# Optimization experiments

Measured on AMD Instinct MI355X. Metric: run time of the kernel, lower is better.

The kernel has to match this reference:

```python
import jax, jax.numpy as jnp
import numpy as np

B, N, D = 1, 768, 256
H = 4
HD = D // H
K = 16
EDGE_DIM = 4
LN_EPS = 1e-5


def setup_inputs() -> dict:
    key = jax.random.key(0)
    ks = jax.random.split(key, 16)
    g = lambda k, shape, fan: jax.random.normal(k, shape, jnp.float32) / np.sqrt(fan)
    return {
        'x': jax.random.normal(ks[0], (B, N, D), jnp.float32),
        'Wqkv_w': g(ks[1], (D, 3 * D), D), 'Wqkv_b': jnp.zeros((3 * D,), jnp.float32),
        'out_w': g(ks[2], (D, D), D), 'out_b': jnp.zeros((D,), jnp.float32),
        'ffn1_w': g(ks[3], (2 * D, 2 * D), 2 * D), 'ffn1_b': jnp.zeros((2 * D,), jnp.float32),
        'ln_g': jnp.ones((2 * D,), jnp.float32), 'ln_b': jnp.zeros((2 * D,), jnp.float32),
        'ffn2_w': g(ks[4], (2 * D, D), 2 * D), 'ffn2_b': jnp.zeros((D,), jnp.float32),
        'e1_w': g(ks[5], (EDGE_DIM, 2 * H), EDGE_DIM), 'e1_b': jnp.zeros((2 * H,), jnp.float32),
        'e2_w': g(ks[6], (2 * H, H), 2 * H), 'e2_b': jnp.zeros((H,), jnp.float32),
        'graph_gate': jnp.float32(0.5),
    }


def _normalize(v):
    return v / jnp.clip(jnp.linalg.norm(v, axis=-1, keepdims=True), 1e-12)


def reference(x, Wqkv_w, Wqkv_b, out_w, out_b, ffn1_w, ffn1_b, ln_g, ln_b,
              ffn2_w, ffn2_b, e1_w, e1_b, e2_w, e2_b, graph_gate):
    b, n, d = x.shape
    # ---- graph topology (no grad, discrete top-k) ----
    xs = jax.lax.stop_gradient(x)
    dn_s = _normalize(xs)
    sim_d = jnp.einsum('bnd,bmd->bnm', dn_s, dn_s)
    eye = jnp.eye(n, dtype=bool)
    sim_d = jnp.where(eye, -jnp.inf, sim_d)
    idx = jax.lax.top_k(sim_d, K)[1]                       # (B,N,K)
    adj = jnp.zeros((b, n, n), bool).at[
        jnp.arange(b)[:, None, None], jnp.arange(n)[None, :, None], idx].set(True)
    adj = adj | jnp.swapaxes(adj, 1, 2) | eye              # symmetric + self loops
    # ---- differentiable edge features (B,N,N,4) ----
    dnm = _normalize(x)
    sim = jnp.einsum('bnd,bmd->bnm', dnm, dnm)
    diff = x[:, :, None, :] - x[:, None, :, :]             # (B,N,N,D) memory-bound
    l2 = jnp.linalg.norm(diff, axis=-1) / np.float32(np.sqrt(d))
    ad = jnp.abs(diff)
    ef = jnp.stack([sim, l2, ad.mean(-1), ad.max(-1)], axis=-1)
    # ---- edge bias per head (B,H,N,N) ----
    h = jax.nn.relu(ef @ e1_w + e1_b)
    bias = jnp.transpose(h @ e2_w + e2_b, (0, 3, 1, 2))
    # ---- attention ----
    qkv = (x @ Wqkv_w + Wqkv_b).reshape(b, n, H, HD, 3)
    qkv = jnp.transpose(qkv, (0, 2, 1, 3, 4))              # (B,H,N,HD,3)
    q, k, v = qkv[..., 0], qkv[..., 1], qkv[..., 2]
    logits = jnp.einsum('bhnd,bhmd->bhnm', q, k) / np.float32(np.sqrt(HD))
    logits = logits + graph_gate * bias
    logits = jnp.where(adj[:, None], logits, -jnp.inf)     # sparse masking
    attn = jax.nn.softmax(logits, axis=-1)
    ctx = jnp.einsum('bhnm,bhmd->bhnd', attn, v)
    msg = jnp.transpose(ctx, (0, 2, 1, 3)).reshape(b, n, d) @ out_w + out_b
    # ---- FFN: Linear -> LayerNorm -> GELU -> Linear, residual ----
    y = jnp.concatenate([x, msg], axis=-1) @ ffn1_w + ffn1_b
    mu = y.mean(-1, keepdims=True)
    var = ((y - mu) ** 2).mean(-1, keepdims=True)
    y = (y - mu) / jnp.sqrt(var + LN_EPS) * ln_g + ln_b
    y = jax.nn.gelu(y, approximate=False)
    return x + (y @ ffn2_w + ffn2_b)
```

## Files before the change

### kernel.cpp

```cpp
#include <hip/hip_runtime.h>
#include <hip/hip_bf16.h>
#include <math.h>

#define NN 768
#define DD 256
#define NHEAD 4
#define HDIM 64
#define TOPK 16

typedef __attribute__((ext_vector_type(8))) short short8;
typedef __attribute__((ext_vector_type(4))) float f32x4;

__device__ __forceinline__ unsigned short f2bf(float f) {
    unsigned u = __float_as_uint(f);
    unsigned r = u + 0x7fffu + ((u >> 16) & 1u);
    return (unsigned short)(r >> 16);
}

__global__ __launch_bounds__(256) void k_prep_norms(
        const float* __restrict__ Wqkv, const float* __restrict__ outw,
        const float* __restrict__ f1w,  const float* __restrict__ f2w,
        unsigned short* __restrict__ t_qkv, unsigned short* __restrict__ t_out,
        unsigned short* __restrict__ t_f1,  unsigned short* __restrict__ t_f2,
        unsigned short* __restrict__ t_g,   unsigned short* __restrict__ t_outn,
        const float* __restrict__ x,
        double* __restrict__ nrm2_d, double* __restrict__ nrm_d,
        double* __restrict__ invn_d,
        unsigned short* __restrict__ xb, unsigned int* __restrict__ adjw) {
    int b = blockIdx.x;
    int tid = threadIdx.x;
    if (b < 640) {
        const float* src; unsigned short* dst; int K, C, tile;
        if (b < 192)      { src = Wqkv; dst = t_qkv; K = 256; C = 768; tile = b; }
        else if (b < 256) { src = outw; dst = t_out; K = 256; C = 256; tile = b - 192; }
        else if (b < 512) { src = f1w;  dst = t_f1;  K = 512; C = 512; tile = b - 256; }
        else              { src = f2w;  dst = t_f2;  K = 512; C = 256; tile = b - 512; }
        int tpr = C / 32;
        int k0 = (tile / tpr) * 32, c0 = (tile % tpr) * 32;
        __shared__ float tls[32][33];
        int r = tid >> 3, c4 = (tid & 7) * 4;
        float4 v = *(const float4*)&src[(size_t)(k0 + r) * C + c0 + c4];
        tls[r][c4 + 0] = v.x; tls[r][c4 + 1] = v.y;
        tls[r][c4 + 2] = v.z; tls[r][c4 + 3] = v.w;
        __syncthreads();
        int rc = tid >> 3, k4 = (tid & 7) * 4;
        unsigned short* d = &dst[(size_t)(c0 + rc) * K + k0 + k4];
        unsigned short w0 = f2bf(tls[k4 + 0][rc]);
        unsigned short w1 = f2bf(tls[k4 + 1][rc]);
        unsigned short w2 = f2bf(tls[k4 + 2][rc]);
        unsigned short w3 = f2bf(tls[k4 + 3][rc]);
        d[0] = w0; d[1] = w1; d[2] = w2; d[3] = w3;
        if (b >= 256 && b < 512 && k0 < 256) {
            unsigned short* d2 = &t_g[(size_t)(c0 + rc) * 512 + k0 + k4];
            d2[0] = w0; d2[1] = w1; d2[2] = w2; d2[3] = w3;
        }
    } else if (b < 832) {
        int nb = b - 640;
        int gid = nb * 256 + tid;
        adjw[gid * 3 + 0] = 0u;
        adjw[gid * 3 + 1] = 0u;
        adjw[gid * 3 + 2] = 0u;
        int n = nb * 4 + (tid >> 6);
        int lane = tid & 63;
        const float* row = x + (size_t)n * DD;
        double s = 0.0;
        #pragma unroll
        for (int i = 0; i < 4; ++i) {
            float v = row[lane + 64 * i];
            xb[(size_t)n * DD + lane + 64 * i] = f2bf(v);
            s += (double)v * (double)v;
        }
        for (int off = 32; off > 0; off >>= 1) s += __shfl_down(s, off);
        if (lane == 0) {
            nrm2_d[n] = s;
            double nv = sqrt(s);
            nrm_d[n] = nv;
            invn_d[n] = 1.0 / fmax(nv, 1e-12);
        }
    } else {
        int idx = (b - 832) * 1024 + tid * 4;
        float4 v = *(const float4*)&outw[idx];
        t_outn[idx + 0] = f2bf(v.x);
        t_outn[idx + 1] = f2bf(v.y);
        t_outn[idx + 2] = f2bf(v.z);
        t_outn[idx + 3] = f2bf(v.w);
    }
}

__global__ __launch_bounds__(512) void k_simqkv(
        const float* __restrict__ x, const double* __restrict__ invn_d,
        double* __restrict__ simd,
        const unsigned short* __restrict__ xbf,
        const unsigned short* __restrict__ t_qkv,
        const float* __restrict__ Wqkv_b,
        float* __restrict__ qb, float* __restrict__ kb, float* __restrict__ vb,
        const unsigned short* __restrict__ t_f1,
        const unsigned short* __restrict__ t_outn,
        unsigned short* __restrict__ t_g,
        const float* __restrict__ out_b, const float* __restrict__ f1w,
        const float* __restrict__ ffn1_b, float* __restrict__ bias_f) {
    __shared__ float A[2][32][68];
    __shared__ float Bm[2][32][68];
    int b = blockIdx.x;
    int tid = threadIdx.x;
    if (b < 300) {
        int r = (int)((sqrtf(8.f * (float)b + 1.f) - 1.f) * 0.5f);
        while ((r + 1) * (r + 2) / 2 <= b) ++r;
        while (r * (r + 1) / 2 > b) --r;
        int c = b - r * (r + 1) / 2;
        int n0 = c * 32, m0 = r * 32;

        int g = tid >> 8;
        int t = tid & 255;
        int tx = t & 15, ty = t >> 4;
        double d00 = 0.0, d01 = 0.0, d10 = 0.0, d11 = 0.0;

        #pragma unroll
        for (int kt = 0; kt < 2; ++kt) {
            int d0 = g * 128 + kt * 64;
            #pragma unroll
            for (int it = 0; it < 8; ++it) {
                int l = t + 256 * it;
                int rr = l >> 6, cc = l & 63;
                A[g][rr][cc]  = x[(size_t)(n0 + rr) * DD + d0 + cc];
                Bm[g][rr][cc] = x[(size_t)(m0 + rr) * DD + d0 + cc];
            }
            __syncthreads();
            for (int d = 0; d < 64; d += 4) {
                float4 b0 = *(const float4*)&Bm[g][tx][d];
                float4 b1 = *(const float4*)&Bm[g][tx + 16][d];
                float4 a0 = *(const float4*)&A[g][ty][d];
                float4 a1 = *(const float4*)&A[g][ty + 16][d];
                double b0x = b0.x, b0y = b0.y, b0z = b0.z, b0w = b0.w;
                double b1x = b1.x, b1y = b1.y, b1z = b1.z, b1w = b1.w;
                double a0x = a0.x, a0y = a0.y, a0z = a0.z, a0w = a0.w;
                double a1x = a1.x, a1y = a1.y, a1z = a1.z, a1w = a1.w;
                d00 += a0x * b0x + a0y * b0y + a0z * b0z + a0w * b0w;
                d01 += a0x * b1x + a0y * b1y + a0z * b1z + a0w * b1w;
                d10 += a1x * b0x + a1y * b0y + a1z * b0z + a1w * b0w;
                d11 += a1x * b1x + a1y * b1y + a1z * b1z + a1w * b1w;
            }
            __syncthreads();
        }

        double* part = (double*)&A[0][0][0];
        if (g == 1) {
            part[t * 4 + 0] = d00; part[t * 4 + 1] = d01;
            part[t * 4 + 2] = d10; part[t * 4 + 3] = d11;
        }
        __syncthreads();
        if (g == 0) {
            d00 += part[t * 4 + 0]; d01 += part[t * 4 + 1];
            d10 += part[t * 4 + 2]; d11 += part[t * 4 + 3];
            double in_m0 = invn_d[m0 + tx], in_m1 = invn_d[m0 + tx + 16];
            double in_n0 = invn_d[n0 + ty], in_n1 = invn_d[n0 + ty + 16];
            double v00 = d00 * in_n0 * in_m0;
            double v01 = d01 * in_n0 * in_m1;
            double v10 = d10 * in_n1 * in_m0;
            double v11 = d11 * in_n1 * in_m1;
            simd[(size_t)(n0 + ty) * NN + m0 + tx]           = v00;
            simd[(size_t)(n0 + ty) * NN + m0 + tx + 16]      = v01;
            simd[(size_t)(n0 + ty + 16) * NN + m0 + tx]      = v10;
            simd[(size_t)(n0 + ty + 16) * NN + m0 + tx + 16] = v11;
            simd[(size_t)(m0 + tx) * NN + n0 + ty]           = v00;
            simd[(size_t)(m0 + tx + 16) * NN + n0 + ty]      = v01;
            simd[(size_t)(m0 + tx) * NN + n0 + ty + 16]      = v10;
            simd[(size_t)(m0 + tx + 16) * NN + n0 + ty + 16] = v11;
        }
    } else if (b < 588) {
        int w = tid >> 6, lane = tid & 63;
        int id = (b - 300) * 8 + w;
        int rt = id % 48, ct = id / 48;
        int m0 = rt * 16, n0 = ct * 16;
        int fr = lane & 15, fg = lane >> 4;
        f32x4 acc = {0.f, 0.f, 0.f, 0.f};
        const unsigned short* brow = &t_qkv[(size_t)(n0 + fr) * DD];
        #pragma unroll
        for (int k0 = 0; k0 < DD; k0 += 32) {
            short8 a = *(const short8*)&xbf[(size_t)(m0 + fr) * DD + k0 + fg * 8];
            short8 bb8 = *(const short8*)&brow[k0 + fg * 8];
            acc = __builtin_amdgcn_mfma_f32_16x16x32_bf16(a, bb8, acc, 0, 0, 0);
        }
        int cidx = n0 + fr;
        int hh = cidx / 192, rem = cidx % 192, hd = rem / 3, s = rem % 3;
        float* dst = (s == 0) ? qb : (s == 1) ? kb : vb;
        float bb = Wqkv_b[cidx];
        #pragma unroll
        for (int r = 0; r < 4; ++r) {
            int n = m0 + fg * 4 + r;
            dst[((size_t)hh * NN + n) * HDIM + hd] = acc[r] + bb;
        }
    } else if (b < 652) {
        int w = tid >> 6, lane = tid & 63;
        int id = (b - 588) * 8 + w;
        int m0 = (id & 31) * 16;
        int n0 = (id >> 5) * 16;
        int fr = lane & 15, fg = lane >> 4;
        f32x4 acc = {0.f, 0.f, 0.f, 0.f};
        const unsigned short* arow = &t_f1[(size_t)(m0 + fr) * 512 + 256];
        const unsigned short* brow = &t_outn[(size_t)(n0 + fr) * 256];
        #pragma unroll
        for (int k0 = 0; k0 < 256; k0 += 32) {
            short8 a = *(const short8*)&arow[k0 + fg * 8];
            short8 bb8 = *(const short8*)&brow[k0 + fg * 8];
            acc = __builtin_amdgcn_mfma_f32_16x16x32_bf16(a, bb8, acc, 0, 0, 0);
        }
        #pragma unroll
        for (int r = 0; r < 4; ++r)
            t_g[(size_t)(m0 + fg * 4 + r) * 512 + 256 + n0 + fr] = f2bf(acc[r]);
    } else {
        float s = ffn1_b[tid];
        for (int c = 0; c < 256; ++c)
            s += out_b[c] * f1w[(size_t)(256 + c) * 512 + tid];
        bias_f[tid] = s;
    }
}

__global__ __launch_bounds__(256) void k_topk(const double* __restrict__ simd,
                                              unsigned char* __restrict__ adj) {
    int tid = threadIdx.x;
    int w = tid >> 6, l = tid & 63;
    int n = blockIdx.x * 4 + w;
    const double* row = simd + (size_t)n * NN;
    double v[12];
    #pragma unroll
    for (int i = 0; i < 12; ++i) {
        int m = l + 64 * i;
        v[i] = (m == n) ? -INFINITY : row[m];
    }
    if (l == 0) adj[(size_t)n * NN + n] = 1;

    for (int itr = 0; itr < TOPK; ++itr) {
        double bv = -INFINITY; int bi = 0x7fffffff;
        #pragma unroll
        for (int i = 0; i < 12; ++i) {
            if (v[i] > bv) { bv = v[i]; bi = l + 64 * i; }
        }
        #pragma unroll
        for (int off = 32; off > 0; off >>= 1) {
            double ov = __shfl_down(bv, off);
            int    oi = __shfl_down(bi, off);
            if (ov > bv || (ov == bv && oi < bi)) { bv = ov; bi = oi; }
        }
        bi = __shfl(bi, 0);
        if ((bi & 63) == l) {
            int slot = bi >> 6;
            #pragma unroll
            for (int i = 0; i < 12; ++i) if (i == slot) v[i] = -INFINITY;
        }
        if (l == 0) {
            adj[(size_t)n * NN + bi] = 1;
            adj[(size_t)bi * NN + n] = 1;
        }
    }
}

__global__ __launch_bounds__(256) void k_edge_attn(
        const float* __restrict__ x,
        const double* __restrict__ nrm2_d,
        const double* __restrict__ nrm_d,
        const double* __restrict__ simd,
        const unsigned char* __restrict__ adj,
        const float* __restrict__ e1_w, const float* __restrict__ e1_b,
        const float* __restrict__ e2_w, const float* __restrict__ e2_b,
        const float* __restrict__ gate_p,
        const float* __restrict__ q, const float* __restrict__ k,
        const float* __restrict__ v,
        unsigned short* __restrict__ ctxb) {
    int n = blockIdx.x;
    int tid = threadIdx.x;
    int w = tid >> 6, l = tid & 63;
    __shared__ unsigned short idxs[NN];
    __shared__ float w_sh[NHEAD][NN];
    __shared__ float ef2s[NN];
    __shared__ float ef3s[NN];
    __shared__ float qsh[NHEAD][HDIM];
    __shared__ int wtot[4];

    int c = 0; int loc[3];
    #pragma unroll
    for (int i = 0; i < 3; ++i) {
        int m = 3 * tid + i;
        if (adj[(size_t)n * NN + m]) loc[c++] = m;
    }
    int pc = c;
    #pragma unroll
    for (int off = 1; off < 64; off <<= 1) {
        int o = __shfl_up(pc, off);
        if (l >= off) pc += o;
    }
    if (l == 63) wtot[w] = pc;
    qsh[w][l] = q[((size_t)w * NN + n) * HDIM + l];
    __syncthreads();
    int base = 0;
    #pragma unroll
    for (int ww = 0; ww < 4; ++ww) if (ww < w) base += wtot[ww];
    int start = base + pc - c;
    for (int i = 0; i < c; ++i) idxs[start + i] = (unsigned short)loc[i];
    int cnt = wtot[0] + wtot[1] + wtot[2] + wtot[3];
    __syncthreads();

    float xa[4];
    #pragma unroll
    for (int i = 0; i < 4; ++i) xa[i] = x[(size_t)n * DD + l + 64 * i];

    for (int j = w; j < cnt; j += 4) {
        int m = idxs[j];
        float sab = 0.f, mab = 0.f;
        #pragma unroll
        for (int i = 0; i < 4; ++i) {
            float xb = x[(size_t)m * DD + l + 64 * i];
            float ad = fabsf(xa[i] - xb);
            sab += ad;
            mab = fmaxf(mab, ad);
        }
        #pragma unroll
        for (int off = 32; off > 0; off >>= 1) {
            sab += __shfl_xor(sab, off);
            mab = fmaxf(mab, __shfl_xor(mab, off));
        }
        if (l == 0) { ef2s[j] = sab * (1.f / 256.f); ef3s[j] = mab; }
    }
    __syncthreads();

    double nrm2n = nrm2_d[n];
    double nrmn  = nrm_d[n];
    float gate = gate_p[0];
    for (int j0 = 0; j0 < cnt; j0 += 64) {
        int j = j0 + (tid >> 2);
        int hh = tid & 3;
        if (j < cnt) {
            int m = idxs[j];
            double s_d   = simd[(size_t)n * NN + m];
            double nrm2m = nrm2_d[m];
            double dotd  = s_d * nrmn * nrm_d[m];
            double l2sq  = fmax(nrm2n + nrm2m - 2.0 * dotd, 0.0);
            float ef0 = (float)s_d;
            float ef1 = (float)(sqrt(l2sq) * (1.0 / 16.0));
            float ef2 = ef2s[j];
            float ef3 = ef3s[j];
            float bb = e2_b[hh];
            #pragma unroll
            for (int jj = 0; jj < 8; ++jj) {
                float hv = e1_b[jj] + ef0 * e1_w[0 * 8 + jj] + ef1 * e1_w[1 * 8 + jj]
                         + ef2 * e1_w[2 * 8 + jj] + ef3 * e1_w[3 * 8 + jj];
                bb += fmaxf(hv, 0.f) * e2_w[jj * 4 + hh];
            }
            w_sh[hh][j] = gate * bb;
        }
    }
    __syncthreads();

    int h = w;
    float lmax = -INFINITY;
    for (int j = l; j < cnt; j += 64) {
        int m = idxs[j];
        const float4* kr = (const float4*)(k + ((size_t)h * NN + m) * HDIM);
        float dotv = 0.f;
        #pragma unroll
        for (int d4 = 0; d4 < HDIM / 4; ++d4) {
            float4 kv = kr[d4];
            dotv += qsh[h][4 * d4 + 0] * kv.x + qsh[h][4 * d4 + 1] * kv.y
                  + qsh[h][4 * d4 + 2] * kv.z + qsh[h][4 * d4 + 3] * kv.w;
        }
        w_sh[h][j] = dotv * 0.125f + w_sh[h][j];
        lmax = fmaxf(lmax, w_sh[h][j]);
    }
    #pragma unroll
    for (int off = 32; off > 0; off >>= 1)
        lmax = fmaxf(lmax, __shfl_xor(lmax, off));

    float lsum = 0.f;
    for (int j = l; j < cnt; j += 64) {
        float e = expf(w_sh[h][j] - lmax);
        w_sh[h][j] = e;
        lsum += e;
    }
    #pragma unroll
    for (int off = 32; off > 0; off >>= 1) lsum += __shfl_xor(lsum, off);
    float inv = 1.f / lsum;
    __syncthreads();

    float acc = 0.f;
    #pragma unroll 4
    for (int j = 0; j < cnt; ++j)
        acc += w_sh[h][j] * v[((size_t)h * NN + idxs[j]) * HDIM + l];
    ctxb[(size_t)n * DD + h * HDIM + l] = f2bf(acc * inv);
}

template<int KD, int MODE, bool CONCAT>
__global__ __launch_bounds__(256) void k_gemm_reg(const unsigned short* __restrict__ A,
                                                  const unsigned short* __restrict__ A2,
                                                  const unsigned short* __restrict__ Bt,
                                                  const float* __restrict__ bias,
                                                  const float* __restrict__ resid,
                                                  float* __restrict__ out,
                                                  unsigned short* __restrict__ outb,
                                                  int ncols) {
    int tid = threadIdx.x;
    int w = tid >> 6, lane = tid & 63;
    int m0 = blockIdx.y * 64 + w * 16;
    int n0 = blockIdx.x * 16;
    int fr = lane & 15, fg = lane >> 4;
    f32x4 acc = {0.f, 0.f, 0.f, 0.f};

    const unsigned short* brow = &Bt[(size_t)(n0 + fr) * KD];
    #pragma unroll
    for (int k0 = 0; k0 < KD; k0 += 32) {
        const unsigned short* Asrc = A; int koff = k0;
        if (CONCAT && k0 >= 256) { Asrc = A2; koff = k0 - 256; }
        int lda = CONCAT ? 256 : KD;
        short8 a = *(const short8*)&Asrc[(size_t)(m0 + fr) * lda + koff + fg * 8];
        short8 b = *(const short8*)&brow[k0 + fg * 8];
        acc = __builtin_amdgcn_mfma_f32_16x16x32_bf16(a, b, acc, 0, 0, 0);
    }

    int cidx = n0 + fr;
    float bb = bias[cidx];
    #pragma unroll
    for (int r = 0; r < 4; ++r) {
        int n = m0 + fg * 4 + r;
        float val = acc[r] + bb;
        if (MODE == 1) val += resid[(size_t)n * ncols + cidx];
        if (MODE == 3) outb[(size_t)n * ncols + cidx] = f2bf(val);
        else           out [(size_t)n * ncols + cidx] = val;
    }
}

__global__ __launch_bounds__(256) void k_ln_gelu(const float* __restrict__ y,
                                                 const float* __restrict__ g,
                                                 const float* __restrict__ b,
                                                 unsigned short* __restrict__ ybb) {
    int n = blockIdx.x;
    int tid = threadIdx.x;
    const float* row = y + (size_t)n * 512;
    __shared__ float red[256];
    float v0 = row[tid], v1 = row[tid + 256];

    red[tid] = v0 + v1; __syncthreads();
    for (int s = 128; s > 0; s >>= 1) {
        if (tid < s) red[tid] += red[tid + s];
        __syncthreads();
    }
    float mu = red[0] * (1.f / 512.f);
    __syncthreads();

    float d0 = v0 - mu, d1 = v1 - mu;
    red[tid] = d0 * d0 + d1 * d1; __syncthreads();
    for (int s = 128; s > 0; s >>= 1) {
        if (tid < s) red[tid] += red[tid + s];
        __syncthreads();
    }
    float var = red[0] * (1.f / 512.f);
    float rstd = 1.f / sqrtf(var + 1e-5f);

    float z0 = d0 * rstd * g[tid] + b[tid];
    float z1 = d1 * rstd * g[tid + 256] + b[tid + 256];
    float o0 = 0.5f * z0 * (1.f + erff(z0 * 0.70710678118654752f));
    float o1 = 0.5f * z1 * (1.f + erff(z1 * 0.70710678118654752f));
    ybb[(size_t)n * 512 + tid]       = f2bf(o0);
    ybb[(size_t)n * 512 + tid + 256] = f2bf(o1);
}

extern "C" void kernel_launch(void* const* d_in, const int* in_sizes, int n_in,
                              void* d_out, int out_size, void* d_ws, size_t ws_size,
                              hipStream_t stream) {
    const float* x       = (const float*)d_in[0];
    const float* Wqkv_w  = (const float*)d_in[1];
    const float* Wqkv_b  = (const float*)d_in[2];
    const float* out_w   = (const float*)d_in[3];
    const float* out_b   = (const float*)d_in[4];
    const float* ffn1_w  = (const float*)d_in[5];
    const float* ffn1_b  = (const float*)d_in[6];
    const float* ln_g    = (const float*)d_in[7];
    const float* ln_b    = (const float*)d_in[8];
    const float* ffn2_w  = (const float*)d_in[9];
    const float* ffn2_b  = (const float*)d_in[10];
    const float* e1_w    = (const float*)d_in[11];
    const float* e1_b    = (const float*)d_in[12];
    const float* e2_w    = (const float*)d_in[13];
    const float* e2_b    = (const float*)d_in[14];
    const float* gate    = (const float*)d_in[15];

    char* base = (char*)d_ws;
    double* simd   = (double*)base;            base += (size_t)NN * NN * 8;
    double* nrm2_d = (double*)base;            base += NN * 8;
    double* nrm_d  = (double*)base;            base += NN * 8;
    double* invn_d = (double*)base;            base += NN * 8;
    float* qb      = (float*)base;             base += (size_t)NN * DD * 4;
    float* kb      = (float*)base;             base += (size_t)NN * DD * 4;
    float* vb      = (float*)base;             base += (size_t)NN * DD * 4;
    float* yb      = (float*)base;             base += (size_t)NN * 512 * 4;
    unsigned char* adj = (unsigned char*)base;  base += (size_t)NN * NN;
    unsigned short* xbf  = (unsigned short*)base; base += (size_t)NN * DD * 2;
    unsigned short* ctxb = (unsigned short*)base; base += (size_t)NN * DD * 2;
    unsigned short* ybb  = (unsigned short*)base; base += (size_t)NN * 512 * 2;
    unsigned short* t_qkv = (unsigned short*)base; base += (size_t)768 * 256 * 2;
    unsigned short* t_out = (unsigned short*)base; base += (size_t)256 * 256 * 2;
    unsigned short* t_f1  = (unsigned short*)base; base += (size_t)512 * 512 * 2;
    unsigned short* t_f2  = (unsigned short*)base; base += (size_t)256 * 512 * 2;
    unsigned short* t_g   = (unsigned short*)base; base += (size_t)512 * 512 * 2;
    unsigned short* t_outn = (unsigned short*)base; base += (size_t)256 * 256 * 2;
    float* bias_f  = (float*)base;             base += 512 * 4;

    k_prep_norms<<<896, 256, 0, stream>>>(Wqkv_w, out_w, ffn1_w, ffn2_w,
                                          t_qkv, t_out, t_f1, t_f2, t_g, t_outn,
                                          x, nrm2_d, nrm_d, invn_d, xbf,
                                          (unsigned int*)adj);

    k_simqkv<<<653, 512, 0, stream>>>(x, invn_d, simd, xbf, t_qkv, Wqkv_b,
                                      qb, kb, vb, t_f1, t_outn, t_g,
                                      out_b, ffn1_w, ffn1_b, bias_f);

    k_topk<<<192, 256, 0, stream>>>(simd, adj);

    k_edge_attn<<<NN, 256, 0, stream>>>(x, nrm2_d, nrm_d, simd, adj,
                                        e1_w, e1_b, e2_w, e2_b, gate,
                                        qb, kb, vb, ctxb);

    k_gemm_reg<512, 0, true><<<dim3(32, 12), 256, 0, stream>>>(
        xbf, ctxb, t_g, bias_f, nullptr, yb, nullptr, 512);

    k_ln_gelu<<<NN, 256, 0, stream>>>(yb, ln_g, ln_b, ybb);

    k_gemm_reg<512, 1, false><<<dim3(16, 12), 256, 0, stream>>>(
        ybb, nullptr, t_f2, ffn2_b, x, (float*)d_out, nullptr, DD);
}
```

Baseline: 74.05 us.

## Fuse LayerNorm+GELU into FFN2 GEMM, drop unused out_w transpose, stage sim tiles as double

The LayerNorm and GELU step is folded into the second FFN GEMM. Each block normalizes its 16 rows of y into shared memory as bf16, then runs MFMA against the transposed ffn2 weights, which removes one kernel launch and the ybb round-trip through global memory. Each block recomputes LN for its rows, and there are 4 column blocks per row group, so the LN work is repeated 4 times. The unused out_w transpose is removed from the prep kernel, and the fp64 similarity tile now stages x already converted to double in shared memory with vectorized float4 loads, at the cost of more LDS traffic per element.

```diff
diff --git a/kernel.cpp b/kernel.cpp
--- a/kernel.cpp
+++ b/kernel.cpp
@@ -18,9 +18,10 @@
 }
 
 __global__ __launch_bounds__(256) void k_prep_norms(
-        const float* __restrict__ Wqkv, const float* __restrict__ outw,
+        const float* __restrict__ Wqkv,
+        const float* __restrict__ outw,
         const float* __restrict__ f1w,  const float* __restrict__ f2w,
-        unsigned short* __restrict__ t_qkv, unsigned short* __restrict__ t_out,
+        unsigned short* __restrict__ t_qkv,
         unsigned short* __restrict__ t_f1,  unsigned short* __restrict__ t_f2,
         unsigned short* __restrict__ t_g,   unsigned short* __restrict__ t_outn,
         const float* __restrict__ x,
@@ -29,12 +30,11 @@
         unsigned short* __restrict__ xb, unsigned int* __restrict__ adjw) {
     int b = blockIdx.x;
     int tid = threadIdx.x;
-    if (b < 640) {
+    if (b < 576) {
         const float* src; unsigned short* dst; int K, C, tile;
         if (b < 192)      { src = Wqkv; dst = t_qkv; K = 256; C = 768; tile = b; }
-        else if (b < 256) { src = outw; dst = t_out; K = 256; C = 256; tile = b - 192; }
-        else if (b < 512) { src = f1w;  dst = t_f1;  K = 512; C = 512; tile = b - 256; }
-        else              { src = f2w;  dst = t_f2;  K = 512; C = 256; tile = b - 512; }
+        else if (b < 448) { src = f1w;  dst = t_f1;  K = 512; C = 512; tile = b - 192; }
+        else              { src = f2w;  dst = t_f2;  K = 512; C = 256; tile = b - 448; }
         int tpr = C / 32;
         int k0 = (tile / tpr) * 32, c0 = (tile % tpr) * 32;
         __shared__ float tls[32][33];
@@ -50,12 +50,12 @@
         unsigned short w2 = f2bf(tls[k4 + 2][rc]);
         unsigned short w3 = f2bf(tls[k4 + 3][rc]);
         d[0] = w0; d[1] = w1; d[2] = w2; d[3] = w3;
-        if (b >= 256 && b < 512 && k0 < 256) {
+        if (b >= 192 && b < 448 && k0 < 256) {
             unsigned short* d2 = &t_g[(size_t)(c0 + rc) * 512 + k0 + k4];
             d2[0] = w0; d2[1] = w1; d2[2] = w2; d2[3] = w3;
         }
-    } else if (b < 832) {
-        int nb = b - 640;
+    } else if (b < 768) {
+        int nb = b - 576;
         int gid = nb * 256 + tid;
         adjw[gid * 3 + 0] = 0u;
         adjw[gid * 3 + 1] = 0u;
@@ -78,7 +78,7 @@
             invn_d[n] = 1.0 / fmax(nv, 1e-12);
         }
     } else {
-        int idx = (b - 832) * 1024 + tid * 4;
+        int idx = (b - 768) * 1024 + tid * 4;
         float4 v = *(const float4*)&outw[idx];
         t_outn[idx + 0] = f2bf(v.x);
         t_outn[idx + 1] = f2bf(v.y);
@@ -99,8 +99,8 @@
         unsigned short* __restrict__ t_g,
         const float* __restrict__ out_b, const float* __restrict__ f1w,
         const float* __restrict__ ffn1_b, float* __restrict__ bias_f) {
-    __shared__ float A[2][32][68];
-    __shared__ float Bm[2][32][68];
+    __shared__ double Ad[2][32][38];
+    __shared__ double Bd[2][32][38];
     int b = blockIdx.x;
     int tid = threadIdx.x;
     if (b < 300) {
@@ -113,28 +113,34 @@
         int g = tid >> 8;
         int t = tid & 255;
         int tx = t & 15, ty = t >> 4;
+        int srow = t >> 3;
+        int skq  = (t & 7) * 4;
         double d00 = 0.0, d01 = 0.0, d10 = 0.0, d11 = 0.0;
 
         #pragma unroll
-        for (int kt = 0; kt < 2; ++kt) {
-            int d0 = g * 128 + kt * 64;
+        for (int ch = 0; ch < 4; ++ch) {
+            int d0 = g * 128 + ch * 32;
+            float4 av = *(const float4*)&x[(size_t)(n0 + srow) * DD + d0 + skq];
+            float4 bv = *(const float4*)&x[(size_t)(m0 + srow) * DD + d0 + skq];
+            Ad[g][srow][skq + 0] = (double)av.x;
+            Ad[g][srow][skq + 1] = (double)av.y;
+            Ad[g][srow][skq + 2] = (double)av.z;
+            Ad[g][srow][skq + 3] = (double)av.w;
+            Bd[g][srow][skq + 0] = (double)bv.x;
+            Bd[g][srow][skq + 1] = (double)bv.y;
+            Bd[g][srow][skq + 2] = (double)bv.z;
+            Bd[g][srow][skq + 3] = (double)bv.w;
+            __syncthreads();
             #pragma unroll
-            for (int it = 0; it < 8; ++it) {
-                int l = t + 256 * it;
-                int rr = l >> 6, cc = l & 63;
-                A[g][rr][cc]  = x[(size_t)(n0 + rr) * DD + d0 + cc];
-                Bm[g][rr][cc] = x[(size_t)(m0 + rr) * DD + d0 + cc];
-            }
-            __syncthreads();
-            for (int d = 0; d < 64; d += 4) {
-                float4 b0 = *(const float4*)&Bm[g][tx][d];
-                float4 b1 = *(const float4*)&Bm[g][tx + 16][d];
-                float4 a0 = *(const float4*)&A[g][ty][d];
-                float4 a1 = *(const float4*)&A[g][ty + 16][d];
-                double b0x = b0.x, b0y = b0.y, b0z = b0.z, b0w = b0.w;
-                double b1x = b1.x, b1y = b1.y, b1z = b1.z, b1w = b1.w;
-                double a0x = a0.x, a0y = a0.y, a0z = a0.z, a0w = a0.w;
-                double a1x = a1.x, a1y = a1.y, a1z = a1.z, a1w = a1.w;
+            for (int d = 0; d < 32; d += 4) {
+                double a0x = Ad[g][ty][d + 0], a0y = Ad[g][ty][d + 1];
+                double a0z = Ad[g][ty][d + 2], a0w = Ad[g][ty][d + 3];
+                double a1x = Ad[g][ty + 16][d + 0], a1y = Ad[g][ty + 16][d + 1];
+                double a1z = Ad[g][ty + 16][d + 2], a1w = Ad[g][ty + 16][d + 3];
+                double b0x = Bd[g][tx][d + 0], b0y = Bd[g][tx][d + 1];
+                double b0z = Bd[g][tx][d + 2], b0w = Bd[g][tx][d + 3];
+                double b1x = Bd[g][tx + 16][d + 0], b1y = Bd[g][tx + 16][d + 1];
+                double b1z = Bd[g][tx + 16][d + 2], b1w = Bd[g][tx + 16][d + 3];
                 d00 += a0x * b0x + a0y * b0y + a0z * b0z + a0w * b0w;
                 d01 += a0x * b1x + a0y * b1y + a0z * b1z + a0w * b1w;
                 d10 += a1x * b0x + a1y * b0y + a1z * b0z + a1w * b0w;
@@ -143,7 +149,7 @@
             __syncthreads();
         }
 
-        double* part = (double*)&A[0][0][0];
+        double* part = &Ad[0][0][0];
         if (g == 1) {
             part[t * 4 + 0] = d00; part[t * 4 + 1] = d01;
             part[t * 4 + 2] = d10; part[t * 4 + 3] = d11;
@@ -427,39 +433,61 @@
     }
 }
 
-__global__ __launch_bounds__(256) void k_ln_gelu(const float* __restrict__ y,
-                                                 const float* __restrict__ g,
-                                                 const float* __restrict__ b,
-                                                 unsigned short* __restrict__ ybb) {
-    int n = blockIdx.x;
+__global__ __launch_bounds__(256) void k_ffn2_ln(
+        const float* __restrict__ yb,
+        const float* __restrict__ ln_g, const float* __restrict__ ln_b,
+        const unsigned short* __restrict__ t_f2,
+        const float* __restrict__ ffn2_b,
+        const float* __restrict__ x, float* __restrict__ outp) {
+    __shared__ unsigned short ysm[16][520];
     int tid = threadIdx.x;
-    const float* row = y + (size_t)n * 512;
-    __shared__ float red[256];
-    float v0 = row[tid], v1 = row[tid + 256];
-
-    red[tid] = v0 + v1; __syncthreads();
-    for (int s = 128; s > 0; s >>= 1) {
-        if (tid < s) red[tid] += red[tid + s];
-        __syncthreads();
-    }
-    float mu = red[0] * (1.f / 512.f);
+    int w = tid >> 6, lane = tid & 63;
+    int m0 = blockIdx.y * 16;
+    int c0 = blockIdx.x * 64 + w * 16;
+    int fr = lane & 15, fg = lane >> 4;
+
+    #pragma unroll
+    for (int rr = 0; rr < 4; ++rr) {
+        int row = w * 4 + rr;
+        const float* yrow = yb + (size_t)(m0 + row) * 512;
+        float vv[8];
+        float s = 0.f;
+        #pragma unroll
+        for (int i = 0; i < 8; ++i) { vv[i] = yrow[lane + 64 * i]; s += vv[i]; }
+        #pragma unroll
+        for (int off = 32; off > 0; off >>= 1) s += __shfl_xor(s, off);
+        float mu = s * (1.f / 512.f);
+        float qs = 0.f;
+        #pragma unroll
+        for (int i = 0; i < 8; ++i) { float d = vv[i] - mu; qs += d * d; }
+        #pragma unroll
+        for (int off = 32; off > 0; off >>= 1) qs += __shfl_xor(qs, off);
+        float rstd = 1.f / sqrtf(qs * (1.f / 512.f) + 1e-5f);
+        #pragma unroll
+        for (int i = 0; i < 8; ++i) {
+            int cidx = lane + 64 * i;
+            float z = (vv[i] - mu) * rstd * ln_g[cidx] + ln_b[cidx];
+            float o = 0.5f * z * (1.f + erff(z * 0.70710678118654752f));
+            ysm[row][cidx] = f2bf(o);
+        }
+    }
     __syncthreads();
 
-    float d0 = v0 - mu, d1 = v1 - mu;
-    red[tid] = d0 * d0 + d1 * d1; __syncthreads();
-    for (int s = 128; s > 0; s >>= 1) {
-        if (tid < s) red[tid] += red[tid + s];
-        __syncthreads();
-    }
-    float var = red[0] * (1.f / 512.f);
-    float rstd = 1.f / sqrtf(var + 1e-5f);
-
-    float z0 = d0 * rstd * g[tid] + b[tid];
-    float z1 = d1 * rstd * g[tid + 256] + b[tid + 256];
-    float o0 = 0.5f * z0 * (1.f + erff(z0 * 0.70710678118654752f));
-    float o1 = 0.5f * z1 * (1.f + erff(z1 * 0.70710678118654752f));
-    ybb[(size_t)n * 512 + tid]       = f2bf(o0);
-    ybb[(size_t)n * 512 + tid + 256] = f2bf(o1);
+    f32x4 acc = {0.f, 0.f, 0.f, 0.f};
+    const unsigned short* brow = &t_f2[(size_t)(c0 + fr) * 512];
+    #pragma unroll
+    for (int k0 = 0; k0 < 512; k0 += 32) {
+        short8 a = *(const short8*)&ysm[fr][k0 + fg * 8];
+        short8 b = *(const short8*)&brow[k0 + fg * 8];
+        acc = __builtin_amdgcn_mfma_f32_16x16x32_bf16(a, b, acc, 0, 0, 0);
+    }
+    int cidx = c0 + fr;
+    float bb = ffn2_b[cidx];
+    #pragma unroll
+    for (int r = 0; r < 4; ++r) {
+        int n = m0 + fg * 4 + r;
+        outp[(size_t)n * DD + cidx] = acc[r] + bb + x[(size_t)n * DD + cidx];
+    }
 }
 
 extern "C" void kernel_launch(void* const* d_in, const int* in_sizes, int n_in,
@@ -494,17 +522,15 @@
     unsigned char* adj = (unsigned char*)base;  base += (size_t)NN * NN;
     unsigned short* xbf  = (unsigned short*)base; base += (size_t)NN * DD * 2;
     unsigned short* ctxb = (unsigned short*)base; base += (size_t)NN * DD * 2;
-    unsigned short* ybb  = (unsigned short*)base; base += (size_t)NN * 512 * 2;
     unsigned short* t_qkv = (unsigned short*)base; base += (size_t)768 * 256 * 2;
-    unsigned short* t_out = (unsigned short*)base; base += (size_t)256 * 256 * 2;
     unsigned short* t_f1  = (unsigned short*)base; base += (size_t)512 * 512 * 2;
     unsigned short* t_f2  = (unsigned short*)base; base += (size_t)256 * 512 * 2;
     unsigned short* t_g   = (unsigned short*)base; base += (size_t)512 * 512 * 2;
     unsigned short* t_outn = (unsigned short*)base; base += (size_t)256 * 256 * 2;
     float* bias_f  = (float*)base;             base += 512 * 4;
 
-    k_prep_norms<<<896, 256, 0, stream>>>(Wqkv_w, out_w, ffn1_w, ffn2_w,
-                                          t_qkv, t_out, t_f1, t_f2, t_g, t_outn,
+    k_prep_norms<<<832, 256, 0, stream>>>(Wqkv_w, out_w, ffn1_w, ffn2_w,
+                                          t_qkv, t_f1, t_f2, t_g, t_outn,
                                           x, nrm2_d, nrm_d, invn_d, xbf,
                                           (unsigned int*)adj);
 
@@ -521,8 +547,6 @@
     k_gemm_reg<512, 0, true><<<dim3(32, 12), 256, 0, stream>>>(
         xbf, ctxb, t_g, bias_f, nullptr, yb, nullptr, 512);
 
-    k_ln_gelu<<<NN, 256, 0, stream>>>(yb, ln_g, ln_b, ybb);
-
-    k_gemm_reg<512, 1, false><<<dim3(16, 12), 256, 0, stream>>>(
-        ybb, nullptr, t_f2, ffn2_b, x, (float*)d_out, nullptr, DD);
-}
+    k_ffn2_ln<<<dim3(4, 48), 256, 0, stream>>>(
+        yb, ln_g, ln_b, t_f2, ffn2_b, x, (float*)d_out);
+}
```

After: 77.67 us. +4.9%, slower.
